# Kernel optimization log

Measured on AMD Instinct MI355X. Metric: run time of the kernel, lower is better.

Reference implementation:

```python
import jax, jax.numpy as jnp
import numpy as np

N = 262144
E = N * 4  # kNN graph with K=4
D = 64

def setup_inputs() -> dict:
    key = jax.random.key(0)
    ks = jax.random.split(key, 16)
    s = 1.0 / np.sqrt(D)
    inp = {
        "x": jax.random.normal(ks[0], (N, D), jnp.float32),
        "edge_index": jax.random.randint(ks[1], (2, E), 0, N, dtype=jnp.int32).astype(jnp.int64),
        "sage_Wl": jax.random.normal(ks[2], (4, D, D), jnp.float32) * s,
        "sage_Wr": jax.random.normal(ks[3], (4, D, D), jnp.float32) * s,
        "sage_b": jnp.zeros((4, D), jnp.float32),
        "gat_W": jax.random.normal(ks[4], (3, D, D), jnp.float32) * s,
        "gat_a_src": jax.random.normal(ks[5], (3, D), jnp.float32) * s,
        "gat_a_dst": jax.random.normal(ks[6], (3, D), jnp.float32) * s,
        "gat_b": jnp.zeros((3, D), jnp.float32),
        "p1_W": jax.random.normal(ks[7], (64, 64), jnp.float32) * s,
        "p1_b": jnp.zeros((64,), jnp.float32),
        "p2_W": jax.random.normal(ks[8], (32, 64), jnp.float32) * s,
        "p2_b": jnp.zeros((32,), jnp.float32),
        "p3_W": jax.random.normal(ks[9], (16, 32), jnp.float32) * (1.0 / np.sqrt(32)),
        "p3_b": jnp.zeros((16,), jnp.float32),
    }
    return inp

def _sage_conv(x, src, dst, Wl, Wr, b, n):
    # mean-aggregate neighbor messages, then lin_l(agg) + lin_r(root)
    msg = x[src]                                               # [E, D]
    ssum = jax.ops.segment_sum(msg, dst, num_segments=n)       # [N, D]
    cnt = jax.ops.segment_sum(jnp.ones((src.shape[0], 1), x.dtype), dst, num_segments=n)
    mean = ssum / jnp.maximum(cnt, 1.0)
    return mean @ Wl.T + x @ Wr.T + b

def _gat_conv(x, src, dst, W, a_src, a_dst, b, n):
    # single-head GATConv with self-loops (PyG defaults)
    h = x @ W.T                                                # [N, D]
    asv = h @ a_src                                            # [N]
    adv = h @ a_dst                                            # [N]
    e = jax.nn.leaky_relu(asv[src] + adv[dst], 0.2)            # [E']
    m = jax.ops.segment_max(e, dst, num_segments=n)
    ee = jnp.exp(e - m[dst])
    denom = jax.ops.segment_sum(ee, dst, num_segments=n)
    alpha = ee / jnp.maximum(denom[dst], 1e-16)
    out = jax.ops.segment_sum(alpha[:, None] * h[src], dst, num_segments=n)
    return out + b

def reference(x, edge_index, sage_Wl, sage_Wr, sage_b,
              gat_W, gat_a_src, gat_a_dst, gat_b,
              p1_W, p1_b, p2_W, p2_b, p3_W, p3_b):
    n = x.shape[0]
    src, dst = edge_index[0], edge_index[1]
    # GraphSAGE: 4 layers, ReLU between layers (not after last)
    h = x
    for i in range(4):
        h = _sage_conv(h, src, dst, sage_Wl[i], sage_Wr[i], sage_b[i], n)
        if i < 3:
            h = jax.nn.relu(h)
    # GAT: 3 layers with self-loops, ReLU between layers
    loop = jnp.arange(n, dtype=src.dtype)
    src_sl = jnp.concatenate([src, loop])
    dst_sl = jnp.concatenate([dst, loop])
    for i in range(3):
        h = _gat_conv(h, src_sl, dst_sl, gat_W[i], gat_a_src[i], gat_a_dst[i], gat_b[i], n)
        if i < 2:
            h = jax.nn.relu(h)
    # ProjectionBlock (dropout inactive at inference)
    h = jax.nn.relu(h @ p1_W.T + p1_b)
    h = jax.nn.relu(h @ p2_W.T + p2_b)
    h = h @ p3_W.T + p3_b
    return h
```

## Files before the change

kernel.cpp:

```cpp
#include <hip/hip_runtime.h>
#include <type_traits>
#include <utility>

typedef __attribute__((ext_vector_type(4))) float f32x4;
typedef __attribute__((ext_vector_type(8))) short short8v;
typedef __attribute__((ext_vector_type(8))) unsigned short ushort8v;
typedef __attribute__((ext_vector_type(8))) __bf16 bf16x8;

template<typename T, typename = void> struct can_mfma : std::false_type {};
template<typename T> struct can_mfma<T, std::void_t<decltype(
  __builtin_amdgcn_mfma_f32_16x16x32_bf16(std::declval<T>(), std::declval<T>(),
                                          std::declval<f32x4>(), 0, 0, 0))>>
  : std::true_type {};
using frag_t = std::conditional_t<can_mfma<short8v>::value, short8v, bf16x8>;

__device__ __forceinline__ f32x4 MFMA(frag_t a, frag_t b, f32x4 c){
  return __builtin_amdgcn_mfma_f32_16x16x32_bf16(a, b, c, 0, 0, 0);
}

__device__ __forceinline__ unsigned short bfrn(float x){
  unsigned u = __float_as_uint(x);
  return (unsigned short)((u + 0x7FFFu + ((u >> 16) & 1u)) >> 16);
}
__device__ __forceinline__ float bf2f(unsigned short h){
  return __uint_as_float(((unsigned)h) << 16);
}
__device__ __forceinline__ float lrelu(float v){ return v > 0.f ? v : 0.2f*v; }
__device__ __forceinline__ void add4(float4& a, const float4 v){
  a.x += v.x; a.y += v.y; a.z += v.z; a.w += v.w; }
__device__ __forceinline__ void fma4(float4& a, float w, const float4 v){
  a.x += w*v.x; a.y += w*v.y; a.z += w*v.z; a.w += w*v.w; }
__device__ __forceinline__ void mul4(float4& a, float w){
  a.x *= w; a.y *= w; a.z *= w; a.w *= w; }

__device__ __forceinline__ void split8(const float* vals, frag_t& fh, frag_t& fl){
  union { unsigned short u[8]; ushort8v v; } Uh, Ul;
#pragma unroll
  for (int j = 0; j < 8; j++){
    unsigned short hb = bfrn(vals[j]);
    Uh.u[j] = hb;
    Ul.u[j] = bfrn(vals[j] - bf2f(hb));
  }
  fh = __builtin_bit_cast(frag_t, Uh.v);
  fl = __builtin_bit_cast(frag_t, Ul.v);
}

__global__ void deg_count(const int* __restrict__ dst, int* __restrict__ deg, int E){
  int e = blockIdx.x*blockDim.x + threadIdx.x;
  if (e < E) atomicAdd(&deg[dst[e]], 1);
}

__global__ void scan_block(const int* __restrict__ deg, int* __restrict__ rowptr,
                           int* __restrict__ bsum){
  __shared__ int s[256];
  int t = threadIdx.x; int i = blockIdx.x*256 + t;
  int v = deg[i];
  s[t] = v; __syncthreads();
  for (int off=1; off<256; off<<=1){
    int a = (t>=off)? s[t-off] : 0; __syncthreads();
    s[t] += a; __syncthreads();
  }
  rowptr[i+1] = s[t];
  if (t==255) bsum[blockIdx.x] = s[255];
}

__global__ void scan_top(int* __restrict__ bsum){
  __shared__ int s[256];
  int t = threadIdx.x;
  int v0=bsum[t*4], v1=bsum[t*4+1], v2=bsum[t*4+2], v3=bsum[t*4+3];
  s[t] = v0+v1+v2+v3; __syncthreads();
  for (int off=1; off<256; off<<=1){
    int a = (t>=off)? s[t-off] : 0; __syncthreads();
    s[t] += a; __syncthreads();
  }
  int excl = (t==0)? 0 : s[t-1];
  bsum[t*4]   = excl;
  bsum[t*4+1] = excl+v0;
  bsum[t*4+2] = excl+v0+v1;
  bsum[t*4+3] = excl+v0+v1+v2;
}

__global__ void scan_add(int* __restrict__ rowptr, const int* __restrict__ bsum){
  int i = blockIdx.x*256 + threadIdx.x;
  rowptr[i+1] += bsum[blockIdx.x];
  if (i == 0) rowptr[0] = 0;
}

__global__ void copy_wp(const int* __restrict__ rowptr, int* __restrict__ wp){
  int i = blockIdx.x*256 + threadIdx.x;
  wp[i] = rowptr[i];
}

__global__ void fill_csr(const int* __restrict__ src, const int* __restrict__ dst,
                         int* __restrict__ wp, int* __restrict__ col, int E){
  int e = blockIdx.x*blockDim.x + threadIdx.x;
  if (e < E){
    int d = dst[e];
    int pos = atomicAdd(&wp[d], 1);
    col[pos] = src[e];
  }
}

__global__ void prep_weights(const float* __restrict__ Wl, const float* __restrict__ Wr,
                             const float* __restrict__ Wg, const float* __restrict__ P1,
                             const float* __restrict__ P2, const float* __restrict__ P3,
                             unsigned short* __restrict__ hi, unsigned short* __restrict__ lo){
  int i = blockIdx.x*256 + threadIdx.x;
  if (i >= 51712) return;
  float v;
  if (i < 16384) v = Wl[i];
  else if (i < 32768) v = Wr[i-16384];
  else if (i < 45056) v = Wg[i-32768];
  else if (i < 49152) v = P1[i-45056];
  else if (i < 51200) v = P2[i-49152];
  else v = P3[i-51200];
  unsigned short hb = bfrn(v);
  hi[i] = hb;
  lo[i] = bfrn(v - bf2f(hb));
}

__global__ void pre_eattn(const int* __restrict__ col, const float* __restrict__ asv,
                          float* __restrict__ eattn, int E){
  int j = blockIdx.x*256 + threadIdx.x;
  if (j < E) eattn[j] = asv[col[j]];
}

__global__ __launch_bounds__(256,3) void sage_mfma(
    const float* __restrict__ cur, const int* __restrict__ rowptr,
    const int* __restrict__ col,
    const unsigned short* __restrict__ WlHi, const unsigned short* __restrict__ WlLo,
    const unsigned short* __restrict__ WrHi, const unsigned short* __restrict__ WrLo,
    const float* __restrict__ bias, float* __restrict__ out, int do_relu){
  __shared__ __align__(16) unsigned short sMhi[64*64];
  __shared__ __align__(16) unsigned short sMlo[64*64];
  __shared__ __align__(16) unsigned short sW[4][64*64/16*16];
  __shared__ int srp[65];
  int t = threadIdx.x;
  int row0 = blockIdx.x * 64;
  if (t < 65) srp[t] = rowptr[row0 + t];
  int w = t >> 6, l = t & 63;
  int lr = l & 15, lg = l >> 4;
  {
    const ushort8v* g0 = (const ushort8v*)WlHi;
    const ushort8v* g1 = (const ushort8v*)WlLo;
    const ushort8v* g2 = (const ushort8v*)WrHi;
    const ushort8v* g3 = (const ushort8v*)WrLo;
#pragma unroll
    for (int i = 0; i < 2; i++){
      int c = t + i*256;
      int row = c >> 3, slot = c & 7;
      int addr = row*64 + ((slot ^ (row & 7)) << 3);
      *(ushort8v*)&sW[0][addr] = g0[c];
      *(ushort8v*)&sW[1][addr] = g1[c];
      *(ushort8v*)&sW[2][addr] = g2[c];
      *(ushort8v*)&sW[3][addr] = g3[c];
    }
  }
  __syncthreads();
  {
    int o = l & 7;
    int rw = l >> 3;
    const float4* base4 = (const float4*)cur;
#pragma unroll
    for (int p = 0; p < 2; p++){
      int r = p*32 + w*8 + rw;
      int beg = srp[r], end = srp[r+1];
      float4 a0 = {0,0,0,0}, a1 = a0;
      for (int j = beg; j < end; j += 4){
        int e1i = end - 1;
        int i1 = j+1 < end ? j+1 : e1i;
        int i2 = j+2 < end ? j+2 : e1i;
        int i3 = j+3 < end ? j+3 : e1i;
        int s0 = col[j], s1 = col[i1], s2 = col[i2], s3 = col[i3];
        float w1 = (j+1<end)?1.f:0.f, w2=(j+2<end)?1.f:0.f, w3=(j+3<end)?1.f:0.f;
        const float4* p0 = base4 + (size_t)s0*16 + o*2;
        const float4* p1 = base4 + (size_t)s1*16 + o*2;
        const float4* p2 = base4 + (size_t)s2*16 + o*2;
        const float4* p3 = base4 + (size_t)s3*16 + o*2;
        float4 q00=p0[0], q01=p0[1], q10=p1[0], q11=p1[1];
        float4 q20=p2[0], q21=p2[1], q30=p3[0], q31=p3[1];
        add4(a0,q00);    add4(a1,q01);
        fma4(a0,w1,q10); fma4(a1,w1,q11);
        fma4(a0,w2,q20); fma4(a1,w2,q21);
        fma4(a0,w3,q30); fma4(a1,w3,q31);
      }
      float rdeg = 1.f / fmaxf((float)(end-beg), 1.f);
      mul4(a0,rdeg); mul4(a1,rdeg);
      float mv[8];
      *(float4*)&mv[0] = a0; *(float4*)&mv[4] = a1;
      union { unsigned short u[8]; ushort8v v; } Uh, Ul;
#pragma unroll
      for (int j2 = 0; j2 < 8; j2++){
        unsigned short hb = bfrn(mv[j2]);
        Uh.u[j2] = hb;
        Ul.u[j2] = bfrn(mv[j2] - bf2f(hb));
      }
      int slot = o ^ (r & 7);
      *(ushort8v*)&sMhi[r*64 + slot*8] = Uh.v;
      *(ushort8v*)&sMlo[r*64 + slot*8] = Ul.v;
    }
  }
  frag_t ax_hi[2], ax_lo[2];
  {
    int grow = row0 + w*16 + lr;
#pragma unroll
    for (int kt = 0; kt < 2; kt++){
      float vals[8];
      const float* p = cur + (size_t)grow*64 + kt*32 + lg*8;
      *(float4*)&vals[0] = *(const float4*)p;
      *(float4*)&vals[4] = *(const float4*)(p + 4);
      split8(vals, ax_hi[kt], ax_lo[kt]);
    }
  }
  __syncthreads();
  int rl = (w << 4) + lr;
  frag_t am_hi[2], am_lo[2];
#pragma unroll
  for (int kt = 0; kt < 2; kt++){
    int slot = (kt*4 + lg) ^ (rl & 7);
    am_hi[kt] = __builtin_bit_cast(frag_t, *(const ushort8v*)&sMhi[rl*64 + slot*8]);
    am_lo[kt] = __builtin_bit_cast(frag_t, *(const ushort8v*)&sMlo[rl*64 + slot*8]);
  }
#pragma unroll
  for (int ct = 0; ct < 4; ct++){
    float bv = bias[ct*16 + lr];
    f32x4 acc = {bv, bv, bv, bv};
    int wrow = ct*16 + lr;
#pragma unroll
    for (int kt = 0; kt < 2; kt++){
      int sl = wrow*64 + (((kt*4 + lg) ^ (wrow & 7)) << 3);
      frag_t blh = __builtin_bit_cast(frag_t, *(const ushort8v*)&sW[0][sl]);
      frag_t bll = __builtin_bit_cast(frag_t, *(const ushort8v*)&sW[1][sl]);
      acc = MFMA(am_hi[kt], blh, acc);
      acc = MFMA(am_lo[kt], blh, acc);
      acc = MFMA(am_hi[kt], bll, acc);
      frag_t brh = __builtin_bit_cast(frag_t, *(const ushort8v*)&sW[2][sl]);
      frag_t brl = __builtin_bit_cast(frag_t, *(const ushort8v*)&sW[3][sl]);
      acc = MFMA(ax_hi[kt], brh, acc);
      acc = MFMA(ax_lo[kt], brh, acc);
      acc = MFMA(ax_hi[kt], brl, acc);
    }
#pragma unroll
    for (int r = 0; r < 4; r++){
      float v = acc[r];
      if (do_relu) v = fmaxf(v, 0.f);
      out[(size_t)(row0 + w*16 + lg*4 + r)*64 + ct*16 + lr] = v;
    }
  }
}

__global__ __launch_bounds__(256,8) void gat_mfma(
    const float* __restrict__ cur,
    const unsigned short* __restrict__ WHi, const unsigned short* __restrict__ WLo,
    const float* __restrict__ a_src, const float* __restrict__ a_dst,
    float* __restrict__ h, float* __restrict__ asv, float* __restrict__ adv){
  __shared__ __align__(16) unsigned short sW[2][64*64];
  int t = threadIdx.x;
  int row0 = blockIdx.x * 64;
  int w = t >> 6, l = t & 63;
  int lr = l & 15, lg = l >> 4;
  {
    const ushort8v* g0 = (const ushort8v*)WHi;
    const ushort8v* g1 = (const ushort8v*)WLo;
#pragma unroll
    for (int i = 0; i < 2; i++){
      int c = t + i*256;
      int row = c >> 3, slot = c & 7;
      int addr = row*64 + ((slot ^ (row & 7)) << 3);
      *(ushort8v*)&sW[0][addr] = g0[c];
      *(ushort8v*)&sW[1][addr] = g1[c];
    }
  }
  frag_t ax_hi[2], ax_lo[2];
  {
    int grow = row0 + w*16 + lr;
#pragma unroll
    for (int kt = 0; kt < 2; kt++){
      float vals[8];
      const float* p = cur + (size_t)grow*64 + kt*32 + lg*8;
      *(float4*)&vals[0] = *(const float4*)p;
      *(float4*)&vals[4] = *(const float4*)(p + 4);
      split8(vals, ax_hi[kt], ax_lo[kt]);
    }
  }
  __syncthreads();
  float pav[4] = {0,0,0,0}, pdv[4] = {0,0,0,0};
#pragma unroll
  for (int ct = 0; ct < 4; ct++){
    f32x4 acc = {0,0,0,0};
    int wrow = ct*16 + lr;
#pragma unroll
    for (int kt = 0; kt < 2; kt++){
      int sl = wrow*64 + (((kt*4 + lg) ^ (wrow & 7)) << 3);
      frag_t bh = __builtin_bit_cast(frag_t, *(const ushort8v*)&sW[0][sl]);
      frag_t bl = __builtin_bit_cast(frag_t, *(const ushort8v*)&sW[1][sl]);
      acc = MFMA(ax_hi[kt], bh, acc);
      acc = MFMA(ax_lo[kt], bh, acc);
      acc = MFMA(ax_hi[kt], bl, acc);
    }
    float asc = a_src[ct*16 + lr], adc = a_dst[ct*16 + lr];
#pragma unroll
    for (int r = 0; r < 4; r++){
      float v = acc[r];
      h[(size_t)(row0 + w*16 + lg*4 + r)*64 + ct*16 + lr] = v;
      pav[r] += v * asc;
      pdv[r] += v * adc;
    }
  }
#pragma unroll
  for (int off = 1; off < 16; off <<= 1){
#pragma unroll
    for (int r = 0; r < 4; r++){
      pav[r] += __shfl_xor(pav[r], off);
      pdv[r] += __shfl_xor(pdv[r], off);
    }
  }
  if (lr == 0){
#pragma unroll
    for (int r = 0; r < 4; r++){
      int row = row0 + w*16 + lg*4 + r;
      asv[row] = pav[r];
      adv[row] = pdv[r];
    }
  }
}

__global__ __launch_bounds__(256,6) void gat_agg(
    const float* __restrict__ h, const int* __restrict__ rowptr,
    const int* __restrict__ col, const float* __restrict__ eattn,
    const float* __restrict__ asv, const float* __restrict__ adv,
    const float* __restrict__ bias, float* __restrict__ out, int do_relu){
  __shared__ int srp[33];
  int t = threadIdx.x;
  int row0 = blockIdx.x * 32;
  if (t < 33) srp[t] = rowptr[row0 + t];
  __syncthreads();
  int rl = t >> 3;
  int o = t & 7;
  int v = row0 + rl;
  int beg = srp[rl], end = srp[rl+1];
  float advv = adv[v];
  float m = lrelu(asv[v] + advv);
  float den = 1.f;
  const float4* hb4 = (const float4*)h;
  const float4* pv = hb4 + (size_t)v*16 + o*2;
  float4 a0 = pv[0], a1 = pv[1];
  for (int j = beg; j < end; j += 4){
    int e1i = end - 1;
    int i1 = j+1 < end ? j+1 : e1i;
    int i2 = j+2 < end ? j+2 : e1i;
    int i3 = j+3 < end ? j+3 : e1i;
    int s0 = col[j], s1 = col[i1], s2 = col[i2], s3 = col[i3];
    float q1 = (j+1<end)?1.f:0.f, q2=(j+2<end)?1.f:0.f, q3=(j+3<end)?1.f:0.f;
    float e0 = lrelu(eattn[j]  + advv);
    float e1 = lrelu(eattn[i1] + advv);
    float e2 = lrelu(eattn[i2] + advv);
    float e3 = lrelu(eattn[i3] + advv);
    float cm = fmaxf(fmaxf(e0, e1), fmaxf(e2, e3));
    if (cm > m){
      float sc = expf(m - cm);
      den *= sc; mul4(a0, sc); mul4(a1, sc);
      m = cm;
    }
    float w0 = expf(e0 - m);
    float w1 = q1 * expf(e1 - m);
    float w2 = q2 * expf(e2 - m);
    float w3 = q3 * expf(e3 - m);
    den += w0 + w1 + w2 + w3;
    const float4* p0 = hb4 + (size_t)s0*16 + o*2;
    const float4* p1 = hb4 + (size_t)s1*16 + o*2;
    const float4* p2 = hb4 + (size_t)s2*16 + o*2;
    const float4* p3 = hb4 + (size_t)s3*16 + o*2;
    float4 g00=p0[0], g01=p0[1], g10=p1[0], g11=p1[1];
    float4 g20=p2[0], g21=p2[1], g30=p3[0], g31=p3[1];
    fma4(a0,w0,g00); fma4(a1,w0,g01);
    fma4(a0,w1,g10); fma4(a1,w1,g11);
    fma4(a0,w2,g20); fma4(a1,w2,g21);
    fma4(a0,w3,g30); fma4(a1,w3,g31);
  }
  float rden = 1.f / fmaxf(den, 1e-16f);
  const float4* b4 = (const float4*)bias;
  float4 bb0 = b4[o*2], bb1 = b4[o*2+1];
  mul4(a0,rden); mul4(a1,rden);
  add4(a0,bb0); add4(a1,bb1);
  if (do_relu){
    a0.x=fmaxf(a0.x,0.f); a0.y=fmaxf(a0.y,0.f); a0.z=fmaxf(a0.z,0.f); a0.w=fmaxf(a0.w,0.f);
    a1.x=fmaxf(a1.x,0.f); a1.y=fmaxf(a1.y,0.f); a1.z=fmaxf(a1.z,0.f); a1.w=fmaxf(a1.w,0.f);
  }
  float4* o4 = (float4*)out + (size_t)v*16 + o*2;
  o4[0] = a0; o4[1] = a1;
}

__global__ __launch_bounds__(256,3) void mlp3(
    const float* __restrict__ in,
    const unsigned short* __restrict__ W1Hi, const unsigned short* __restrict__ W1Lo,
    const unsigned short* __restrict__ W2Hi, const unsigned short* __restrict__ W2Lo,
    const unsigned short* __restrict__ W3Hi, const unsigned short* __restrict__ W3Lo,
    const float* __restrict__ b1, const float* __restrict__ b2,
    const float* __restrict__ b3, float* __restrict__ out){
  __shared__ __align__(16) unsigned short sW1[2][4096];
  __shared__ __align__(16) unsigned short sW2[2][2048];
  __shared__ __align__(16) unsigned short sW3[2][512];
  __shared__ float sH1[64*68];
  __shared__ float sH2[64*36];
  int t = threadIdx.x;
  int row0 = blockIdx.x * 64;
  int w = t >> 6, l = t & 63;
  int lr = l & 15, lg = l >> 4;
  {
#pragma unroll
    for (int i = 0; i < 2; i++){
      int c = t + i*256;
      int row = c >> 3, slot = c & 7;
      int addr = row*64 + ((slot ^ (row & 7)) << 3);
      *(ushort8v*)&sW1[0][addr] = ((const ushort8v*)W1Hi)[c];
      *(ushort8v*)&sW1[1][addr] = ((const ushort8v*)W1Lo)[c];
    }
    {
      int c = t;
      int row = c >> 3, slot = c & 7;
      int addr = row*64 + ((slot ^ (row & 7)) << 3);
      *(ushort8v*)&sW2[0][addr] = ((const ushort8v*)W2Hi)[c];
      *(ushort8v*)&sW2[1][addr] = ((const ushort8v*)W2Lo)[c];
    }
    if (t < 64){
      int row = t >> 2, slot = t & 3;
      int addr = row*32 + ((slot ^ (row & 3)) << 3);
      *(ushort8v*)&sW3[0][addr] = ((const ushort8v*)W3Hi)[t];
      *(ushort8v*)&sW3[1][addr] = ((const ushort8v*)W3Lo)[t];
    }
  }
  frag_t ax_hi[2], ax_lo[2];
  {
    int grow = row0 + w*16 + lr;
#pragma unroll
    for (int kt = 0; kt < 2; kt++){
      float vals[8];
      const float* p = in + (size_t)grow*64 + kt*32 + lg*8;
      *(float4*)&vals[0] = *(const float4*)p;
      *(float4*)&vals[4] = *(const float4*)(p + 4);
      split8(vals, ax_hi[kt], ax_lo[kt]);
    }
  }
  __syncthreads();
#pragma unroll
  for (int ct = 0; ct < 4; ct++){
    int wrow = ct*16 + lr;
    float bv = b1[wrow];
    f32x4 acc = {bv, bv, bv, bv};
#pragma unroll
    for (int kt = 0; kt < 2; kt++){
      int sl = wrow*64 + (((kt*4 + lg) ^ (wrow & 7)) << 3);
      frag_t bh = __builtin_bit_cast(frag_t, *(const ushort8v*)&sW1[0][sl]);
      frag_t bl = __builtin_bit_cast(frag_t, *(const ushort8v*)&sW1[1][sl]);
      acc = MFMA(ax_hi[kt], bh, acc);
      acc = MFMA(ax_lo[kt], bh, acc);
      acc = MFMA(ax_hi[kt], bl, acc);
    }
#pragma unroll
    for (int r = 0; r < 4; r++)
      sH1[(w*16 + lg*4 + r)*68 + wrow] = fmaxf(acc[r], 0.f);
  }
  frag_t a2_hi[2], a2_lo[2];
#pragma unroll
  for (int kt = 0; kt < 2; kt++){
    float vals[8];
    const float* p = &sH1[(w*16 + lr)*68 + kt*32 + lg*8];
    *(float4*)&vals[0] = *(const float4*)p;
    *(float4*)&vals[4] = *(const float4*)(p + 4);
    split8(vals, a2_hi[kt], a2_lo[kt]);
  }
#pragma unroll
  for (int ct = 0; ct < 2; ct++){
    int wrow = ct*16 + lr;
    float bv = b2[wrow];
    f32x4 acc = {bv, bv, bv, bv};
#pragma unroll
    for (int kt = 0; kt < 2; kt++){
      int sl = wrow*64 + (((kt*4 + lg) ^ (wrow & 7)) << 3);
      frag_t bh = __builtin_bit_cast(frag_t, *(const ushort8v*)&sW2[0][sl]);
      frag_t bl = __builtin_bit_cast(frag_t, *(const ushort8v*)&sW2[1][sl]);
      acc = MFMA(a2_hi[kt], bh, acc);
      acc = MFMA(a2_lo[kt], bh, acc);
      acc = MFMA(a2_hi[kt], bl, acc);
    }
#pragma unroll
    for (int r = 0; r < 4; r++)
      sH2[(w*16 + lg*4 + r)*36 + wrow] = fmaxf(acc[r], 0.f);
  }
  frag_t a3_hi, a3_lo;
  {
    float vals[8];
    const float* p = &sH2[(w*16 + lr)*36 + lg*8];
    *(float4*)&vals[0] = *(const float4*)p;
    *(float4*)&vals[4] = *(const float4*)(p + 4);
    split8(vals, a3_hi, a3_lo);
  }
  {
    float bv = b3[lr];
    f32x4 acc = {bv, bv, bv, bv};
    int sl = lr*32 + ((lg ^ (lr & 3)) << 3);
    frag_t bh = __builtin_bit_cast(frag_t, *(const ushort8v*)&sW3[0][sl]);
    frag_t bl = __builtin_bit_cast(frag_t, *(const ushort8v*)&sW3[1][sl]);
    acc = MFMA(a3_hi, bh, acc);
    acc = MFMA(a3_lo, bh, acc);
    acc = MFMA(a3_hi, bl, acc);
#pragma unroll
    for (int r = 0; r < 4; r++)
      out[(size_t)(row0 + w*16 + lg*4 + r)*16 + lr] = acc[r];
  }
}

extern "C" void kernel_launch(void* const* d_in, const int* in_sizes, int n_in,
                              void* d_out, int out_size, void* d_ws, size_t ws_size,
                              hipStream_t stream) {
    const float* x        = (const float*)d_in[0];
    const int*   ei       = (const int*)d_in[1];
    const float* sage_Wl  = (const float*)d_in[2];
    const float* sage_Wr  = (const float*)d_in[3];
    const float* sage_b   = (const float*)d_in[4];
    const float* gat_W    = (const float*)d_in[5];
    const float* gat_as   = (const float*)d_in[6];
    const float* gat_ad   = (const float*)d_in[7];
    const float* gat_b    = (const float*)d_in[8];
    const float* p1W = (const float*)d_in[9],  *p1b = (const float*)d_in[10];
    const float* p2W = (const float*)d_in[11], *p2b = (const float*)d_in[12];
    const float* p3W = (const float*)d_in[13], *p3b = (const float*)d_in[14];

    int n = in_sizes[0] / 64;
    int E = in_sizes[1] / 2;
    const int* src = ei;
    const int* dst = ei + E;

    size_t N64 = (size_t)n * 64;
    float* bufA   = (float*)d_ws;
    float* bufB   = bufA + N64;
    int*   rowptr = (int*)(bufB + N64);
    int*   wp     = rowptr + (n + 4);
    int*   col    = wp + n;
    int*   bsum   = col + E;
    float* asv    = (float*)(bsum + 1024);
    float* adv    = asv + n;
    float* eattn  = adv + n;

    unsigned short* whi = (unsigned short*)wp;
    unsigned short* wlo = whi + 51712;

    int nb = n / 256;

    hipMemsetAsync(wp, 0, (size_t)n * 4, stream);
    deg_count<<<(E + 255) / 256, 256, 0, stream>>>(dst, wp, E);
    scan_block<<<nb, 256, 0, stream>>>(wp, rowptr, bsum);
    scan_top<<<1, 256, 0, stream>>>(bsum);
    scan_add<<<nb, 256, 0, stream>>>(rowptr, bsum);
    copy_wp<<<nb, 256, 0, stream>>>(rowptr, wp);
    fill_csr<<<(E + 255) / 256, 256, 0, stream>>>(src, dst, wp, col, E);

    prep_weights<<<202, 256, 0, stream>>>(sage_Wl, sage_Wr, gat_W, p1W, p2W, p3W,
                                          whi, wlo);

    const float* cur = x;
    float* nxt = bufA;
    for (int l = 0; l < 4; l++){
        sage_mfma<<<n / 64, 256, 0, stream>>>(cur, rowptr, col,
            whi + l*4096,          wlo + l*4096,
            whi + 16384 + l*4096,  wlo + 16384 + l*4096,
            sage_b + l*64, nxt, l < 3 ? 1 : 0);
        cur = nxt;
        nxt = (nxt == bufA) ? bufB : bufA;
    }

    for (int l = 0; l < 3; l++){
        gat_mfma<<<n / 64, 256, 0, stream>>>(cur,
            whi + 32768 + l*4096, wlo + 32768 + l*4096,
            gat_as + l*64, gat_ad + l*64, nxt, asv, adv);
        pre_eattn<<<(E + 255) / 256, 256, 0, stream>>>(col, asv, eattn, E);
        gat_agg<<<n / 32, 256, 0, stream>>>(nxt, rowptr, col, eattn, asv, adv,
            gat_b + l*64, (float*)cur, l < 2 ? 1 : 0);
    }

    mlp3<<<n / 64, 256, 0, stream>>>(cur,
        whi + 45056, wlo + 45056,
        whi + 49152, wlo + 49152,
        whi + 51200, wlo + 51200,
        p1b, p2b, p3b, (float*)d_out);
}
```

Measured before the change: 664.8 us.

## Fold attention gather into GAT aggregation and merge CSR scan kernels

Removes the separate pre_eattn kernel and its edge-sized buffer by gathering asv[src] directly inside gat_agg. It fuses scan_add with the copy into the write-pointer array and uses a nontemporal store when filling CSR columns. The shared-memory staging of rowptr and its barrier are replaced by direct global reads. Together these cut kernel launches and memory round trips, at the cost of more scattered gathers in the aggregation loop.

```diff
diff --git a/kernel.cpp b/kernel.cpp
--- a/kernel.cpp
+++ b/kernel.cpp
@@ -80,15 +80,13 @@
   bsum[t*4+3] = excl+v0+v1+v2;
 }
 
-__global__ void scan_add(int* __restrict__ rowptr, const int* __restrict__ bsum){
+__global__ void scan_add_wp(int* __restrict__ rowptr, int* __restrict__ wp,
+                            const int* __restrict__ bsum){
   int i = blockIdx.x*256 + threadIdx.x;
-  rowptr[i+1] += bsum[blockIdx.x];
-  if (i == 0) rowptr[0] = 0;
-}
-
-__global__ void copy_wp(const int* __restrict__ rowptr, int* __restrict__ wp){
-  int i = blockIdx.x*256 + threadIdx.x;
-  wp[i] = rowptr[i];
+  int v = rowptr[i+1] + bsum[blockIdx.x];
+  rowptr[i+1] = v;
+  wp[i+1] = v;
+  if (i == 0){ rowptr[0] = 0; wp[0] = 0; }
 }
 
 __global__ void fill_csr(const int* __restrict__ src, const int* __restrict__ dst,
@@ -97,7 +95,7 @@
   if (e < E){
     int d = dst[e];
     int pos = atomicAdd(&wp[d], 1);
-    col[pos] = src[e];
+    __builtin_nontemporal_store(src[e], &col[pos]);
   }
 }
 
@@ -119,12 +117,6 @@
   lo[i] = bfrn(v - bf2f(hb));
 }
 
-__global__ void pre_eattn(const int* __restrict__ col, const float* __restrict__ asv,
-                          float* __restrict__ eattn, int E){
-  int j = blockIdx.x*256 + threadIdx.x;
-  if (j < E) eattn[j] = asv[col[j]];
-}
-
 __global__ __launch_bounds__(256,3) void sage_mfma(
     const float* __restrict__ cur, const int* __restrict__ rowptr,
     const int* __restrict__ col,
@@ -133,11 +125,9 @@
     const float* __restrict__ bias, float* __restrict__ out, int do_relu){
   __shared__ __align__(16) unsigned short sMhi[64*64];
   __shared__ __align__(16) unsigned short sMlo[64*64];
-  __shared__ __align__(16) unsigned short sW[4][64*64/16*16];
-  __shared__ int srp[65];
+  __shared__ __align__(16) unsigned short sW[4][4096];
   int t = threadIdx.x;
   int row0 = blockIdx.x * 64;
-  if (t < 65) srp[t] = rowptr[row0 + t];
   int w = t >> 6, l = t & 63;
   int lr = l & 15, lg = l >> 4;
   {
@@ -156,7 +146,6 @@
       *(ushort8v*)&sW[3][addr] = g3[c];
     }
   }
-  __syncthreads();
   {
     int o = l & 7;
     int rw = l >> 3;
@@ -164,7 +153,8 @@
 #pragma unroll
     for (int p = 0; p < 2; p++){
       int r = p*32 + w*8 + rw;
-      int beg = srp[r], end = srp[r+1];
+      int row = row0 + r;
+      int beg = rowptr[row], end = rowptr[row+1];
       float4 a0 = {0,0,0,0}, a1 = a0;
       for (int j = beg; j < end; j += 4){
         int e1i = end - 1;
@@ -254,7 +244,7 @@
     const unsigned short* __restrict__ WHi, const unsigned short* __restrict__ WLo,
     const float* __restrict__ a_src, const float* __restrict__ a_dst,
     float* __restrict__ h, float* __restrict__ asv, float* __restrict__ adv){
-  __shared__ __align__(16) unsigned short sW[2][64*64];
+  __shared__ __align__(16) unsigned short sW[2][4096];
   int t = threadIdx.x;
   int row0 = blockIdx.x * 64;
   int w = t >> 6, l = t & 63;
@@ -327,18 +317,15 @@
 
 __global__ __launch_bounds__(256,6) void gat_agg(
     const float* __restrict__ h, const int* __restrict__ rowptr,
-    const int* __restrict__ col, const float* __restrict__ eattn,
-    const float* __restrict__ asv, const float* __restrict__ adv,
-    const float* __restrict__ bias, float* __restrict__ out, int do_relu){
-  __shared__ int srp[33];
+    const int* __restrict__ col, const float* __restrict__ asv,
+    const float* __restrict__ adv, const float* __restrict__ bias,
+    float* __restrict__ out, int do_relu){
   int t = threadIdx.x;
   int row0 = blockIdx.x * 32;
-  if (t < 33) srp[t] = rowptr[row0 + t];
-  __syncthreads();
   int rl = t >> 3;
   int o = t & 7;
   int v = row0 + rl;
-  int beg = srp[rl], end = srp[rl+1];
+  int beg = rowptr[v], end = rowptr[v+1];
   float advv = adv[v];
   float m = lrelu(asv[v] + advv);
   float den = 1.f;
@@ -352,10 +339,10 @@
     int i3 = j+3 < end ? j+3 : e1i;
     int s0 = col[j], s1 = col[i1], s2 = col[i2], s3 = col[i3];
     float q1 = (j+1<end)?1.f:0.f, q2=(j+2<end)?1.f:0.f, q3=(j+3<end)?1.f:0.f;
-    float e0 = lrelu(eattn[j]  + advv);
-    float e1 = lrelu(eattn[i1] + advv);
-    float e2 = lrelu(eattn[i2] + advv);
-    float e3 = lrelu(eattn[i3] + advv);
+    float e0 = lrelu(asv[s0] + advv);
+    float e1 = lrelu(asv[s1] + advv);
+    float e2 = lrelu(asv[s2] + advv);
+    float e3 = lrelu(asv[s3] + advv);
     float cm = fmaxf(fmaxf(e0, e1), fmaxf(e2, e3));
     if (cm > m){
       float sc = expf(m - cm);
@@ -537,13 +524,12 @@
     float* bufB   = bufA + N64;
     int*   rowptr = (int*)(bufB + N64);
     int*   wp     = rowptr + (n + 4);
-    int*   col    = wp + n;
+    int*   col    = wp + (n + 4);
     int*   bsum   = col + E;
     float* asv    = (float*)(bsum + 1024);
     float* adv    = asv + n;
-    float* eattn  = adv + n;
-
-    unsigned short* whi = (unsigned short*)wp;
+
+    unsigned short* whi = (unsigned short*)(adv + n);
     unsigned short* wlo = whi + 51712;
 
     int nb = n / 256;
@@ -552,8 +538,7 @@
     deg_count<<<(E + 255) / 256, 256, 0, stream>>>(dst, wp, E);
     scan_block<<<nb, 256, 0, stream>>>(wp, rowptr, bsum);
     scan_top<<<1, 256, 0, stream>>>(bsum);
-    scan_add<<<nb, 256, 0, stream>>>(rowptr, bsum);
-    copy_wp<<<nb, 256, 0, stream>>>(rowptr, wp);
+    scan_add_wp<<<nb, 256, 0, stream>>>(rowptr, wp, bsum);
     fill_csr<<<(E + 255) / 256, 256, 0, stream>>>(src, dst, wp, col, E);
 
     prep_weights<<<202, 256, 0, stream>>>(sage_Wl, sage_Wr, gat_W, p1W, p2W, p3W,
@@ -574,8 +559,7 @@
         gat_mfma<<<n / 64, 256, 0, stream>>>(cur,
             whi + 32768 + l*4096, wlo + 32768 + l*4096,
             gat_as + l*64, gat_ad + l*64, nxt, asv, adv);
-        pre_eattn<<<(E + 255) / 256, 256, 0, stream>>>(col, asv, eattn, E);
-        gat_agg<<<n / 32, 256, 0, stream>>>(nxt, rowptr, col, eattn, asv, adv,
+        gat_agg<<<n / 32, 256, 0, stream>>>(nxt, rowptr, col, asv, adv,
             gat_b + l*64, (float*)cur, l < 2 ? 1 : 0);
     }
 
```

New measurement: 668.5 us. No clear change (+0.6%).
